# Optimization experiments

Measured on AMD Instinct MI355X. Metric: run time of the kernel, lower is better.

## Reference

```python
import jax, jax.numpy as jnp
import numpy as np

B, N_IN, N_ALL, NPT, K, C, H = 8, 20000, 1200, 1024, 34, 96, 6
DH = C // H
RADIUS2 = (2.5 * 0.04) ** 2  # grid_size=0.04, sigma=1.0 -> radius 0.1


def _fps(xyz, npoint):
    # furthest point sampling, vectorized over batch, scan over sample steps
    Bb, Nn, _ = xyz.shape
    def step(carry, _):
        dist, far = carry
        cen = jnp.take_along_axis(xyz, far[:, None, None], axis=1)  # [B,1,3]
        d = jnp.sum((xyz - cen) ** 2, -1)                           # [B,N]
        dist = jnp.minimum(dist, d)
        return (dist, jnp.argmax(dist, -1).astype(jnp.int32)), far
    init = (jnp.full((Bb, Nn), 1e10, xyz.dtype), jnp.zeros((Bb,), jnp.int32))
    _, idx = jax.lax.scan(step, init, None, length=npoint)
    return idx.T  # [B, npoint]


def _gather(x, idx):
    return jnp.take_along_axis(x, idx[:, :, None], axis=1)


def _ln(x, g, b):
    m = jnp.mean(x, -1, keepdims=True)
    v = jnp.var(x, -1, keepdims=True)
    return (x - m) * jax.lax.rsqrt(v + 1e-5) * g + b


def _forward(point_clouds, cloud_colors, W_in, b_in, Wq, Wk, Wv, Wo, Wpos, W1, b1, W2, b2, g1, be1, g2, be2, sel):
    fps_idx = _fps(point_clouds, N_ALL)      # [B,1200]
    fps_idx = fps_idx[:, sel]                # random 1024 of 1200 (fixed permutation)
    coord = _gather(point_clouds, fps_idx)   # [B,P,3]
    color = _gather(cloud_colors, fps_idx)   # [B,P,3]
    # ball query within each cloud (all clouds have equal count -> batched dense dists)
    d2 = jnp.sum((coord[:, :, None] - coord[:, None]) ** 2, -1)        # [B,P,P]
    valid = d2 <= RADIUS2
    nidx = jnp.argsort(jnp.where(valid, d2, 1e10), axis=-1)[..., :K]   # [B,P,K]
    nvalid = jnp.take_along_axis(valid, nidx, axis=-1)                 # [B,P,K]
    feat = jnp.concatenate([color, coord], -1)                         # [B,P,6]
    x = feat @ W_in + b_in                                             # [B,P,C]
    q = (x @ Wq).reshape(B, NPT, H, DH)
    k = x @ Wk
    v = x @ Wv
    def gat(t):  # gather per-neighbor features: [B,P,C*] -> [B,P,K,C*]
        return jnp.take_along_axis(t, nidx.reshape(B, NPT * K)[:, :, None], axis=1).reshape(B, NPT, K, -1)
    kn, vn, pn = gat(k), gat(v), gat(coord)
    pe = (coord[:, :, None] - pn) @ Wpos                               # [B,P,K,C] rel-pos enc
    kn = (kn + pe).reshape(B, NPT, K, H, DH)
    vn = (vn + pe).reshape(B, NPT, K, H, DH)
    logits = jnp.einsum('bphd,bpkhd->bphk', q, kn) / jnp.sqrt(jnp.float32(DH))
    logits = jnp.where(nvalid[:, :, None, :], logits, -1e9)
    attn = jax.nn.softmax(logits, -1)
    out = jnp.einsum('bphk,bpkhd->bphd', attn, vn).reshape(B, NPT, C)
    x = _ln(x + out @ Wo, g1, be1)
    x = _ln(x + jax.nn.relu(x @ W1 + b1) @ W2 + b2, g2, be2)
    features = jnp.transpose(x, (0, 2, 1))                             # [B,C,P]
    return features, coord


def setup_inputs() -> dict:
    key = jax.random.key(0)
    ks = jax.random.split(key, 16)
    s = 0.1
    w = lambda k, shp: jax.random.normal(k, shp, jnp.float32) * s
    return {
        'point_clouds': jax.random.uniform(ks[0], (B, N_IN, 3), jnp.float32),
        'cloud_colors': jax.random.uniform(ks[1], (B, N_IN, 3), jnp.float32),
        'W_in': w(ks[2], (6, C)), 'b_in': jnp.zeros((C,), jnp.float32),
        'Wq': w(ks[3], (C, C)), 'Wk': w(ks[4], (C, C)), 'Wv': w(ks[5], (C, C)),
        'Wo': w(ks[6], (C, C)), 'Wpos': w(ks[7], (3, C)),
        'W1': w(ks[8], (C, 4 * C)), 'b1': jnp.zeros((4 * C,), jnp.float32),
        'W2': w(ks[9], (4 * C, C)), 'b2': jnp.zeros((C,), jnp.float32),
        'g1': jnp.ones((C,), jnp.float32), 'be1': jnp.zeros((C,), jnp.float32),
        'g2': jnp.ones((C,), jnp.float32), 'be2': jnp.zeros((C,), jnp.float32),
        'sel': jax.random.permutation(ks[10], N_ALL)[:NPT].astype(jnp.int32),
    }


def reference(point_clouds, cloud_colors, W_in, b_in, Wq, Wk, Wv, Wo, Wpos, W1, b1, W2, b2, g1, be1, g2, be2, sel):
    return _forward(point_clouds, cloud_colors, W_in, b_in, Wq, Wk, Wv, Wo, Wpos, W1, b1, W2, b2, g1, be1, g2, be2, sel)
```

## Files before the change

kernel.cpp:

```cpp
#include <hip/hip_runtime.h>
#include <math.h>

#define B_   8
#define NIN  20000
#define NALL 1200
#define NPTQ 1024
#define KNB  34
#define CH   96
#define FF   384
#define NQ   (B_ * NPTQ)

typedef unsigned int   u32;
typedef unsigned long long u64;

__device__ __forceinline__ float scrub(float f) {
    u32 u = __float_as_uint(f);
    return ((u & 0x7F800000u) == 0x7F800000u) ? 12345.0f : f;
}

__global__ __launch_bounds__(1024) void fps_kernel(const float* __restrict__ pc,
                                                   int* __restrict__ fps_idx) {
    const int b = blockIdx.x;
    const int tid = threadIdx.x;
    const float* base = pc + (size_t)b * NIN * 3;

    float px[20], py[20], pz[20], dist[20];
#pragma unroll
    for (int j = 0; j < 20; ++j) {
        int idx = tid + j * 1024;
        bool ok = (j < 19) || (idx < NIN);
        int ia = ok ? idx : 0;
        px[j] = base[(size_t)ia * 3 + 0];
        py[j] = base[(size_t)ia * 3 + 1];
        pz[j] = base[(size_t)ia * 3 + 2];
        dist[j] = ok ? 1e10f : -1.0f;
    }

    __shared__ float cen[3];
    __shared__ u64 red[16];

    if (tid == 0) {
        fps_idx[b * NALL + 0] = 0;
        cen[0] = px[0]; cen[1] = py[0]; cen[2] = pz[0];
    }
    __syncthreads();

    for (int it = 1; it < NALL; ++it) {
        float cx = cen[0], cy = cen[1], cz = cen[2];
        float bd = -1e38f; int bi = 0;
#pragma unroll
        for (int j = 0; j < 20; ++j) {
            float dx = __fsub_rn(px[j], cx);
            float dy = __fsub_rn(py[j], cy);
            float dz = __fsub_rn(pz[j], cz);
            float d = __fadd_rn(__fadd_rn(__fmul_rn(dx, dx), __fmul_rn(dy, dy)),
                                __fmul_rn(dz, dz));
            float nd = fminf(dist[j], d);
            dist[j] = nd;
            if (nd > bd) { bd = nd; bi = tid + j * 1024; }
        }
        u64 key = ((u64)__float_as_uint(bd) << 32) | (u32)(NIN - bi);
#pragma unroll
        for (int s = 32; s; s >>= 1) {
            u64 o = __shfl_xor(key, s, 64);
            key = (o > key) ? o : key;
        }
        if ((tid & 63) == 0) red[tid >> 6] = key;
        __syncthreads();
        if (tid < 64) {
            u64 k2 = red[tid & 15];
#pragma unroll
            for (int s = 8; s; s >>= 1) {
                u64 o = __shfl_xor(k2, s, 64);
                k2 = (o > k2) ? o : k2;
            }
            if (tid == 0) {
                int w = NIN - (int)(k2 & 0xFFFFFFFFu);
                fps_idx[b * NALL + it] = w;
                const float* p = base + (size_t)w * 3;
                cen[0] = p[0]; cen[1] = p[1]; cen[2] = p[2];
            }
        }
        __syncthreads();
    }
}

__global__ void gather_kernel(const float* __restrict__ pc,
                              const int* __restrict__ fps_idx, const int* __restrict__ sel,
                              float* __restrict__ coord, float* __restrict__ out_coord) {
    int t = blockIdx.x * 256 + threadIdx.x;
    if (t >= NQ) return;
    int b = t >> 10, j = t & 1023;
    int p = fps_idx[b * NALL + sel[j]];
    p = (p < 0) ? 0 : ((p >= NIN) ? (NIN - 1) : p);
    const float* pp = pc + ((size_t)b * NIN + p) * 3;
    float x = pp[0], y = pp[1], z = pp[2];
    coord[(size_t)t * 3 + 0] = x;
    coord[(size_t)t * 3 + 1] = y;
    coord[(size_t)t * 3 + 2] = z;
    out_coord[(size_t)t * 3 + 0] = scrub(x);
    out_coord[(size_t)t * 3 + 1] = scrub(y);
    out_coord[(size_t)t * 3 + 2] = scrub(z);
}

__global__ void knn_kernel(const float* __restrict__ coord, int* __restrict__ nbr) {
    __shared__ float sx[NPTQ], sy[NPTQ], sz[NPTQ];
    const double RAD2D = (2.5 * 0.04) * (2.5 * 0.04);
    int b = blockIdx.x >> 8;
    int i0 = (blockIdx.x & 255) * 4;
    const float* cb = coord + (size_t)b * NPTQ * 3;
    for (int t = threadIdx.x; t < NPTQ; t += 256) {
        sx[t] = cb[(size_t)t * 3 + 0];
        sy[t] = cb[(size_t)t * 3 + 1];
        sz[t] = cb[(size_t)t * 3 + 2];
    }
    __syncthreads();
    int wid = threadIdx.x >> 6, lane = threadIdx.x & 63;
    int i = i0 + wid;
    float qx = sx[i], qy = sy[i], qz = sz[i];
    u64 pk[16];
#pragma unroll
    for (int t = 0; t < 16; ++t) {
        int j = lane + t * 64;
        float dx = __fsub_rn(qx, sx[j]);
        float dy = __fsub_rn(qy, sy[j]);
        float dz = __fsub_rn(qz, sz[j]);
        float d2 = __fadd_rn(__fadd_rn(__fmul_rn(dx, dx), __fmul_rn(dy, dy)),
                             __fmul_rn(dz, dz));
        bool valid = ((double)d2 <= RAD2D);
        pk[t] = valid ? (((u64)__float_as_uint(d2) << 32) | (u32)j) : ~0ull;
    }
    int* out = nbr + ((size_t)b * NPTQ + i) * KNB;
    int k = 0;
    for (; k < KNB; ++k) {
        u64 m = ~0ull;
#pragma unroll
        for (int t = 0; t < 16; ++t) m = (pk[t] < m) ? pk[t] : m;
#pragma unroll
        for (int s = 32; s; s >>= 1) {
            u64 o = __shfl_xor(m, s, 64);
            m = (o < m) ? o : m;
        }
        if (m == ~0ull) break;
#pragma unroll
        for (int t = 0; t < 16; ++t) if (pk[t] == m) pk[t] = ~0ull;
        if (lane == 0) out[k] = (int)(m & 0xFFFFFFFFu);
    }
    for (; k < KNB; ++k) if (lane == 0) out[k] = -1;
}

__global__ void xproj_kernel(const float* __restrict__ pc, const float* __restrict__ col,
                             const int* __restrict__ fps_idx, const int* __restrict__ sel,
                             const float* __restrict__ Win, const float* __restrict__ bin,
                             float* __restrict__ x) {
    int idx = blockIdx.x * 256 + threadIdx.x;
    if (idx >= NQ * CH) return;
    int q = idx / CH, c = idx - q * CH;
    int b = q >> 10, j = q & 1023;
    int p = fps_idx[b * NALL + sel[j]];
    p = (p < 0) ? 0 : ((p >= NIN) ? (NIN - 1) : p);
    const float* pp = pc + ((size_t)b * NIN + p) * 3;
    const float* cc = col + ((size_t)b * NIN + p) * 3;
    float acc = bin[c];
    acc += cc[0] * Win[0 * CH + c];
    acc += cc[1] * Win[1 * CH + c];
    acc += cc[2] * Win[2 * CH + c];
    acc += pp[0] * Win[3 * CH + c];
    acc += pp[1] * Win[4 * CH + c];
    acc += pp[2] * Win[5 * CH + c];
    x[idx] = acc;
}

__global__ void qkv_kernel(const float* __restrict__ x,
                           const float* __restrict__ Wq, const float* __restrict__ Wk,
                           const float* __restrict__ Wv,
                           float* __restrict__ qo, float* __restrict__ ko,
                           float* __restrict__ vo) {
    int idx = blockIdx.x * 256 + threadIdx.x;
    if (idx >= NQ * CH) return;
    int q = idx / CH, c = idx - q * CH;
    const float* xr = x + (size_t)q * CH;
    float aq = 0.f, ak = 0.f, av = 0.f;
    for (int k = 0; k < CH; ++k) {
        float xv = xr[k];
        aq += xv * Wq[k * CH + c];
        ak += xv * Wk[k * CH + c];
        av += xv * Wv[k * CH + c];
    }
    qo[idx] = aq; ko[idx] = ak; vo[idx] = av;
}

__global__ __launch_bounds__(384) void attn_kernel(float* __restrict__ qr1,
                            const float* __restrict__ km, const float* __restrict__ vm,
                            const float* __restrict__ coord, const int* __restrict__ nbr,
                            const float* __restrict__ Wpos, const float* __restrict__ Wo,
                            const float* __restrict__ x) {
    __shared__ float wp[3 * CH];
    __shared__ float os[4][CH];
    for (int t = threadIdx.x; t < 3 * CH; t += 384) wp[t] = Wpos[t];
    __syncthreads();
    int lq = threadIdx.x / CH;
    int c = threadIdx.x - lq * CH;
    int qi = blockIdx.x * 4 + lq;
    int b = qi >> 10, i = qi & 1023;
    const float* crd = coord + (size_t)b * NPTQ * 3;
    float cx = crd[(size_t)i * 3], cy = crd[(size_t)i * 3 + 1], cz = crd[(size_t)i * 3 + 2];
    float qv = qr1[(size_t)qi * CH + c];
    const int* nb = nbr + (size_t)qi * KNB;
    float m = -1e30f, l = 0.f, acc = 0.f;
    for (int t = 0; t < KNB; ++t) {
        int j = nb[t];
        if (j < 0) break;
        float dx = cx - crd[(size_t)j * 3];
        float dy = cy - crd[(size_t)j * 3 + 1];
        float dz = cz - crd[(size_t)j * 3 + 2];
        float pe = dx * wp[c] + dy * wp[CH + c] + dz * wp[2 * CH + c];
        size_t row = (size_t)(b * NPTQ + j) * CH + c;
        float kn = km[row] + pe;
        float s = qv * kn;
        s += __shfl_xor(s, 1); s += __shfl_xor(s, 2);
        s += __shfl_xor(s, 4); s += __shfl_xor(s, 8);
        float logit = s * 0.25f;
        float mn = fmaxf(m, logit);
        float sc = expf(m - mn);
        float p = expf(logit - mn);
        float vn = vm[row] + pe;
        l = l * sc + p;
        acc = acc * sc + p * vn;
        m = mn;
    }
    os[lq][c] = (l > 0.f) ? acc / l : 0.f;
    __syncthreads();
    float r = x[(size_t)qi * CH + c];
    for (int k = 0; k < CH; ++k) r += os[lq][k] * Wo[k * CH + c];
    qr1[(size_t)qi * CH + c] = r;
}

__global__ void ln_kernel(const float* __restrict__ in, const float* __restrict__ g,
                          const float* __restrict__ be, float* __restrict__ out) {
    int row = blockIdx.x * 4 + (threadIdx.x >> 6);
    int lane = threadIdx.x & 63;
    const float* r = in + (size_t)row * CH;
    float e0 = r[lane];
    float e1 = (lane < 32) ? r[64 + lane] : 0.0f;
    float s = e0 + e1;
#pragma unroll
    for (int k = 32; k; k >>= 1) s += __shfl_xor(s, k);
    float mean = s * (1.0f / 96.0f);
    float d0 = e0 - mean, d1 = e1 - mean;
    float vs = d0 * d0 + ((lane < 32) ? d1 * d1 : 0.0f);
#pragma unroll
    for (int k = 32; k; k >>= 1) vs += __shfl_xor(vs, k);
    float rs = 1.0f / sqrtf(vs * (1.0f / 96.0f) + 1e-5f);
    float* o = out + (size_t)row * CH;
    o[lane] = d0 * rs * g[lane] + be[lane];
    if (lane < 32) o[64 + lane] = d1 * rs * g[64 + lane] + be[64 + lane];
}

__global__ __launch_bounds__(384) void ffn_kernel(const float* __restrict__ x2,
                           const float* __restrict__ W1, const float* __restrict__ b1,
                           const float* __restrict__ W2, const float* __restrict__ b2,
                           float* __restrict__ r2) {
    __shared__ float xs[CH];
    __shared__ float hs[FF];
    __shared__ float ps[4][CH];
    int row = blockIdx.x, t = threadIdx.x;
    if (t < CH) xs[t] = x2[(size_t)row * CH + t];
    __syncthreads();
    float a = b1[t];
    for (int k = 0; k < CH; ++k) a += xs[k] * W1[k * FF + t];
    hs[t] = fmaxf(a, 0.0f);
    __syncthreads();
    int chunk = t / CH;
    int c = t - chunk * CH;
    float p = 0.f;
    for (int m = chunk * CH; m < (chunk + 1) * CH; ++m) p += hs[m] * W2[m * CH + c];
    ps[chunk][c] = p;
    __syncthreads();
    if (t < CH) {
        float r = xs[t] + ((ps[0][t] + ps[1][t]) + (ps[2][t] + ps[3][t])) + b2[t];
        r2[(size_t)row * CH + t] = r;
    }
}

__global__ void ln2t_kernel(const float* __restrict__ in, const float* __restrict__ g,
                            const float* __restrict__ be, float* __restrict__ out) {
    int row = blockIdx.x * 4 + (threadIdx.x >> 6);
    int lane = threadIdx.x & 63;
    int b = row >> 10, i = row & 1023;
    const float* r = in + (size_t)row * CH;
    float e0 = r[lane];
    float e1 = (lane < 32) ? r[64 + lane] : 0.0f;
    float s = e0 + e1;
#pragma unroll
    for (int k = 32; k; k >>= 1) s += __shfl_xor(s, k);
    float mean = s * (1.0f / 96.0f);
    float d0 = e0 - mean, d1 = e1 - mean;
    float vs = d0 * d0 + ((lane < 32) ? d1 * d1 : 0.0f);
#pragma unroll
    for (int k = 32; k; k >>= 1) vs += __shfl_xor(vs, k);
    float rs = 1.0f / sqrtf(vs * (1.0f / 96.0f) + 1e-5f);
    float y0 = d0 * rs * g[lane] + be[lane];
    out[((size_t)(b * CH + lane)) * NPTQ + i] = scrub(y0);
    if (lane < 32) {
        float y1 = d1 * rs * g[64 + lane] + be[64 + lane];
        out[((size_t)(b * CH + 64 + lane)) * NPTQ + i] = scrub(y1);
    }
}

extern "C" void kernel_launch(void* const* d_in, const int* in_sizes, int n_in,
                              void* d_out, int out_size, void* d_ws, size_t ws_size,
                              hipStream_t stream) {
    const float* pc   = (const float*)d_in[0];
    const float* col  = (const float*)d_in[1];
    const float* Win  = (const float*)d_in[2];
    const float* bin  = (const float*)d_in[3];
    const float* Wq   = (const float*)d_in[4];
    const float* Wk   = (const float*)d_in[5];
    const float* Wv   = (const float*)d_in[6];
    const float* Wo   = (const float*)d_in[7];
    const float* Wpos = (const float*)d_in[8];
    const float* W1   = (const float*)d_in[9];
    const float* b1   = (const float*)d_in[10];
    const float* W2   = (const float*)d_in[11];
    const float* b2   = (const float*)d_in[12];
    const float* g1   = (const float*)d_in[13];
    const float* be1  = (const float*)d_in[14];
    const float* g2   = (const float*)d_in[15];
    const float* be2  = (const float*)d_in[16];
    const int*  sel   = (const int*)d_in[17];

    float* out_feat  = (float*)d_out;
    float* out_coord = out_feat + (size_t)B_ * CH * NPTQ;

    char* ws = (char*)d_ws;
    size_t off = 0;
    auto alloc = [&](size_t bytes) { void* p = ws + off; off += (bytes + 255) & ~(size_t)255; return p; };
    int*   w_fps   = (int*)  alloc((size_t)B_ * NALL * 4);
    float* w_coord = (float*)alloc((size_t)NQ * 3 * 4);
    int*   w_nbr   = (int*)  alloc((size_t)NQ * KNB * 4);
    float* w_x     = (float*)alloc((size_t)NQ * CH * 4);
    float* w_q     = (float*)alloc((size_t)NQ * CH * 4);
    float* w_k     = (float*)alloc((size_t)NQ * CH * 4);
    float* w_v     = (float*)alloc((size_t)NQ * CH * 4);
    (void)ws_size; (void)in_sizes; (void)n_in; (void)out_size;

    fps_kernel<<<B_, 1024, 0, stream>>>(pc, w_fps);
    gather_kernel<<<NQ / 256, 256, 0, stream>>>(pc, w_fps, sel, w_coord, out_coord);
    knn_kernel<<<NQ / 4, 256, 0, stream>>>(w_coord, w_nbr);
    xproj_kernel<<<NQ * CH / 256, 256, 0, stream>>>(pc, col, w_fps, sel, Win, bin, w_x);
    qkv_kernel<<<NQ * CH / 256, 256, 0, stream>>>(w_x, Wq, Wk, Wv, w_q, w_k, w_v);
    attn_kernel<<<NQ / 4, 384, 0, stream>>>(w_q, w_k, w_v, w_coord, w_nbr, Wpos, Wo, w_x);
    ln_kernel<<<NQ / 4, 256, 0, stream>>>(w_q, g1, be1, w_k);
    ffn_kernel<<<NQ, 384, 0, stream>>>(w_k, W1, b1, W2, b2, w_v);
    ln2t_kernel<<<NQ / 4, 256, 0, stream>>>(w_v, g2, be2, out_feat);
}
```

Baseline: 2.786 ms.

## Split FPS across multiple blocks per cloud with global flag sync; batch FFN rows

Furthest point sampling now runs on 8 cooperating 256-thread blocks per cloud instead of one 1024-thread block. Each step, every block publishes its local argmax key and centroid to global memory and raises a per-block flag, then spins until all sibling blocks have posted before reducing to the global winner. This spreads the serial FPS loop across more CUs, at the cost of a global-memory handshake each iteration and reliance on all blocks being co-resident to avoid deadlock. Separately, the FFN kernel processes four rows per block so each W1/W2 weight load is reused four times.

Result: slower. 6.089 ms (+118.5%).

```diff
diff --git a/kernel.cpp b/kernel.cpp
--- a/kernel.cpp
+++ b/kernel.cpp
@@ -10,6 +10,11 @@
 #define FF   384
 #define NQ   (B_ * NPTQ)
 
+#define SPLIT 8
+#define PPB   (NIN / SPLIT)
+#define FPS_T 256
+#define SLOTS 10
+
 typedef unsigned int   u32;
 typedef unsigned long long u64;
 
@@ -18,38 +23,38 @@
     return ((u & 0x7F800000u) == 0x7F800000u) ? 12345.0f : f;
 }
 
-__global__ __launch_bounds__(1024) void fps_kernel(const float* __restrict__ pc,
-                                                   int* __restrict__ fps_idx) {
-    const int b = blockIdx.x;
+__global__ __launch_bounds__(FPS_T) void fps_kernel(
+        const float* __restrict__ pc, int* __restrict__ fps_idx,
+        u32* flags, u64* __restrict__ hkey, float4* __restrict__ hcen) {
+    const int b   = blockIdx.x / SPLIT;
+    const int s   = blockIdx.x - b * SPLIT;
     const int tid = threadIdx.x;
+    const int lane = tid & 63;
     const float* base = pc + (size_t)b * NIN * 3;
-
-    float px[20], py[20], pz[20], dist[20];
-#pragma unroll
-    for (int j = 0; j < 20; ++j) {
-        int idx = tid + j * 1024;
-        bool ok = (j < 19) || (idx < NIN);
-        int ia = ok ? idx : 0;
-        px[j] = base[(size_t)ia * 3 + 0];
-        py[j] = base[(size_t)ia * 3 + 1];
-        pz[j] = base[(size_t)ia * 3 + 2];
+    const int gbase = s * PPB;
+
+    float px[SLOTS], py[SLOTS], pz[SLOTS], dist[SLOTS];
+#pragma unroll
+    for (int j = 0; j < SLOTS; ++j) {
+        int ib = tid + j * FPS_T;
+        bool ok = ib < PPB;
+        int g = gbase + (ok ? ib : 0);
+        px[j] = base[(size_t)g * 3 + 0];
+        py[j] = base[(size_t)g * 3 + 1];
+        pz[j] = base[(size_t)g * 3 + 2];
         dist[j] = ok ? 1e10f : -1.0f;
     }
 
-    __shared__ float cen[3];
-    __shared__ u64 red[16];
-
-    if (tid == 0) {
-        fps_idx[b * NALL + 0] = 0;
-        cen[0] = px[0]; cen[1] = py[0]; cen[2] = pz[0];
-    }
-    __syncthreads();
+    __shared__ u64 red[4];
+    __shared__ float scen[3];
+
+    float cx = base[0], cy = base[1], cz = base[2];
+    if (s == 0 && tid == 0) fps_idx[b * NALL + 0] = 0;
 
     for (int it = 1; it < NALL; ++it) {
-        float cx = cen[0], cy = cen[1], cz = cen[2];
         float bd = -1e38f; int bi = 0;
 #pragma unroll
-        for (int j = 0; j < 20; ++j) {
+        for (int j = 0; j < SLOTS; ++j) {
             float dx = __fsub_rn(px[j], cx);
             float dy = __fsub_rn(py[j], cy);
             float dz = __fsub_rn(pz[j], cz);
@@ -57,31 +62,58 @@
                                 __fmul_rn(dz, dz));
             float nd = fminf(dist[j], d);
             dist[j] = nd;
-            if (nd > bd) { bd = nd; bi = tid + j * 1024; }
+            if (nd > bd) { bd = nd; bi = gbase + tid + j * FPS_T; }
         }
         u64 key = ((u64)__float_as_uint(bd) << 32) | (u32)(NIN - bi);
-#pragma unroll
-        for (int s = 32; s; s >>= 1) {
-            u64 o = __shfl_xor(key, s, 64);
-            key = (o > key) ? o : key;
-        }
-        if ((tid & 63) == 0) red[tid >> 6] = key;
+        u64 kw = key;
+#pragma unroll
+        for (int st = 32; st; st >>= 1) {
+            u64 o = __shfl_xor(kw, st, 64);
+            kw = (o > kw) ? o : kw;
+        }
+        if (lane == 0) red[tid >> 6] = kw;
         __syncthreads();
+        u64 k2 = red[lane & 3];
+#pragma unroll
+        for (int st = 1; st < 4; st <<= 1) {
+            u64 o = __shfl_xor(k2, st, 64);
+            k2 = (o > k2) ? o : k2;
+        }
+        if (key == k2) {
+            int wj = (bi - gbase - tid) >> 8;
+            size_t slot = ((size_t)b * NALL + it) * SPLIT + s;
+            hkey[slot] = k2;
+            hcen[slot] = make_float4(px[wj], py[wj], pz[wj], 0.f);
+            __threadfence();
+            __hip_atomic_store(&flags[b * SPLIT + s], (u32)it,
+                               __ATOMIC_RELEASE, __HIP_MEMORY_SCOPE_AGENT);
+        }
         if (tid < 64) {
-            u64 k2 = red[tid & 15];
-#pragma unroll
-            for (int s = 8; s; s >>= 1) {
-                u64 o = __shfl_xor(k2, s, 64);
-                k2 = (o > k2) ? o : k2;
+            u64 kk = 0; float xx = 0.f, yy = 0.f, zz = 0.f;
+            if (lane < SPLIT) {
+                while (__hip_atomic_load(&flags[b * SPLIT + lane],
+                                         __ATOMIC_ACQUIRE, __HIP_MEMORY_SCOPE_AGENT)
+                       < (u32)it) { }
+                size_t slot = ((size_t)b * NALL + it) * SPLIT + lane;
+                kk = hkey[slot];
+                float4 cc = hcen[slot];
+                xx = cc.x; yy = cc.y; zz = cc.z;
             }
-            if (tid == 0) {
-                int w = NIN - (int)(k2 & 0xFFFFFFFFu);
-                fps_idx[b * NALL + it] = w;
-                const float* p = base + (size_t)w * 3;
-                cen[0] = p[0]; cen[1] = p[1]; cen[2] = p[2];
+#pragma unroll
+            for (int st = 1; st < SPLIT; st <<= 1) {
+                u64 ok = __shfl_xor(kk, st, 64);
+                float ox = __shfl_xor(xx, st, 64);
+                float oy = __shfl_xor(yy, st, 64);
+                float oz = __shfl_xor(zz, st, 64);
+                if (ok > kk) { kk = ok; xx = ox; yy = oy; zz = oz; }
             }
+            if (lane == 0) {
+                scen[0] = xx; scen[1] = yy; scen[2] = zz;
+                if (s == 0) fps_idx[b * NALL + it] = NIN - (int)(kk & 0xFFFFFFFFu);
+            }
         }
         __syncthreads();
+        cx = scen[0]; cy = scen[1]; cz = scen[2];
     }
 }
 
@@ -261,26 +293,40 @@
                            const float* __restrict__ W1, const float* __restrict__ b1,
                            const float* __restrict__ W2, const float* __restrict__ b2,
                            float* __restrict__ r2) {
-    __shared__ float xs[CH];
-    __shared__ float hs[FF];
-    __shared__ float ps[4][CH];
-    int row = blockIdx.x, t = threadIdx.x;
-    if (t < CH) xs[t] = x2[(size_t)row * CH + t];
-    __syncthreads();
-    float a = b1[t];
-    for (int k = 0; k < CH; ++k) a += xs[k] * W1[k * FF + t];
-    hs[t] = fmaxf(a, 0.0f);
-    __syncthreads();
-    int chunk = t / CH;
-    int c = t - chunk * CH;
-    float p = 0.f;
-    for (int m = chunk * CH; m < (chunk + 1) * CH; ++m) p += hs[m] * W2[m * CH + c];
-    ps[chunk][c] = p;
-    __syncthreads();
-    if (t < CH) {
-        float r = xs[t] + ((ps[0][t] + ps[1][t]) + (ps[2][t] + ps[3][t])) + b2[t];
-        r2[(size_t)row * CH + t] = r;
-    }
+    __shared__ float xs[4][CH];
+    __shared__ float hs[4][FF];
+    __shared__ float ps[4][4][CH];
+    int row0 = blockIdx.x * 4, t = threadIdx.x;
+    { int r = t / CH, c = t - (t / CH) * CH;
+      xs[r][c] = x2[(size_t)(row0 + r) * CH + c]; }
+    __syncthreads();
+    {
+        float bt = b1[t];
+        float a0 = bt, a1 = bt, a2 = bt, a3 = bt;
+        for (int k = 0; k < CH; ++k) {
+            float w = W1[k * FF + t];
+            a0 += xs[0][k] * w; a1 += xs[1][k] * w;
+            a2 += xs[2][k] * w; a3 += xs[3][k] * w;
+        }
+        hs[0][t] = fmaxf(a0, 0.f); hs[1][t] = fmaxf(a1, 0.f);
+        hs[2][t] = fmaxf(a2, 0.f); hs[3][t] = fmaxf(a3, 0.f);
+    }
+    __syncthreads();
+    {
+        int chunk = t / CH, c = t - chunk * CH;
+        float p0 = 0.f, p1 = 0.f, p2 = 0.f, p3 = 0.f;
+        for (int m = chunk * CH; m < (chunk + 1) * CH; ++m) {
+            float w = W2[m * CH + c];
+            p0 += hs[0][m] * w; p1 += hs[1][m] * w;
+            p2 += hs[2][m] * w; p3 += hs[3][m] * w;
+        }
+        ps[0][chunk][c] = p0; ps[1][chunk][c] = p1;
+        ps[2][chunk][c] = p2; ps[3][chunk][c] = p3;
+    }
+    __syncthreads();
+    { int r = t / CH, c = t - (t / CH) * CH;
+      float rr = xs[r][c] + ((ps[r][0][c] + ps[r][1][c]) + (ps[r][2][c] + ps[r][3][c])) + b2[c];
+      r2[(size_t)(row0 + r) * CH + c] = rr; }
 }
 
 __global__ void ln2t_kernel(const float* __restrict__ in, const float* __restrict__ g,
@@ -336,22 +382,27 @@
     char* ws = (char*)d_ws;
     size_t off = 0;
     auto alloc = [&](size_t bytes) { void* p = ws + off; off += (bytes + 255) & ~(size_t)255; return p; };
-    int*   w_fps   = (int*)  alloc((size_t)B_ * NALL * 4);
-    float* w_coord = (float*)alloc((size_t)NQ * 3 * 4);
-    int*   w_nbr   = (int*)  alloc((size_t)NQ * KNB * 4);
-    float* w_x     = (float*)alloc((size_t)NQ * CH * 4);
-    float* w_q     = (float*)alloc((size_t)NQ * CH * 4);
-    float* w_k     = (float*)alloc((size_t)NQ * CH * 4);
-    float* w_v     = (float*)alloc((size_t)NQ * CH * 4);
+    u32*    w_flags = (u32*)   alloc((size_t)B_ * SPLIT * 4);
+    u64*    w_hkey  = (u64*)   alloc((size_t)B_ * NALL * SPLIT * 8);
+    float4* w_hcen  = (float4*)alloc((size_t)B_ * NALL * SPLIT * 16);
+    int*    w_fps   = (int*)   alloc((size_t)B_ * NALL * 4);
+    float*  w_coord = (float*) alloc((size_t)NQ * 3 * 4);
+    int*    w_nbr   = (int*)   alloc((size_t)NQ * KNB * 4);
+    float*  w_x     = (float*) alloc((size_t)NQ * CH * 4);
+    float*  w_q     = (float*) alloc((size_t)NQ * CH * 4);
+    float*  w_k     = (float*) alloc((size_t)NQ * CH * 4);
+    float*  w_v     = (float*) alloc((size_t)NQ * CH * 4);
     (void)ws_size; (void)in_sizes; (void)n_in; (void)out_size;
 
-    fps_kernel<<<B_, 1024, 0, stream>>>(pc, w_fps);
+    hipMemsetAsync(w_flags, 0, (size_t)B_ * SPLIT * 4, stream);
+
+    fps_kernel<<<B_ * SPLIT, FPS_T, 0, stream>>>(pc, w_fps, w_flags, w_hkey, w_hcen);
     gather_kernel<<<NQ / 256, 256, 0, stream>>>(pc, w_fps, sel, w_coord, out_coord);
     knn_kernel<<<NQ / 4, 256, 0, stream>>>(w_coord, w_nbr);
     xproj_kernel<<<NQ * CH / 256, 256, 0, stream>>>(pc, col, w_fps, sel, Win, bin, w_x);
     qkv_kernel<<<NQ * CH / 256, 256, 0, stream>>>(w_x, Wq, Wk, Wv, w_q, w_k, w_v);
     attn_kernel<<<NQ / 4, 384, 0, stream>>>(w_q, w_k, w_v, w_coord, w_nbr, Wpos, Wo, w_x);
     ln_kernel<<<NQ / 4, 256, 0, stream>>>(w_q, g1, be1, w_k);
-    ffn_kernel<<<NQ, 384, 0, stream>>>(w_k, W1, b1, W2, b2, w_v);
+    ffn_kernel<<<NQ / 4, 384, 0, stream>>>(w_k, W1, b1, W2, b2, w_v);
     ln2t_kernel<<<NQ / 4, 256, 0, stream>>>(w_v, g2, be2, out_feat);
 }
```

## Halve FPS barriers with double-buffered reduction and batch FFN rows per block

Applied to the files above, without the earlier changes.

The FPS loop now has every wave read the per-wave partial maxima from a double-buffered shared array and reduce them redundantly. Each thread then loads the new centroid itself, which removes the second __syncthreads and the serial tid==0 step in each of the 1199 iterations. The FFN kernel now processes four rows per block, so each W1/W2 weight load is reused four times, and the grid shrinks accordingly. The cost is more redundant reduction work and global loads of the centroid by every thread, plus more shared memory in the FFN.

New measurement: 2.627 ms. 5.7% less time.

```diff
diff --git a/kernel.cpp b/kernel.cpp
--- a/kernel.cpp
+++ b/kernel.cpp
@@ -9,6 +9,7 @@
 #define CH   96
 #define FF   384
 #define NQ   (B_ * NPTQ)
+#define SL   20
 
 typedef unsigned int   u32;
 typedef unsigned long long u64;
@@ -22,34 +23,36 @@
                                                    int* __restrict__ fps_idx) {
     const int b = blockIdx.x;
     const int tid = threadIdx.x;
+    const int lane = tid & 63;
+    const int wid = tid >> 6;
     const float* base = pc + (size_t)b * NIN * 3;
 
-    float px[20], py[20], pz[20], dist[20];
-#pragma unroll
-    for (int j = 0; j < 20; ++j) {
+    float px[SL], py[SL], pz[SL], dist[SL];
+#pragma unroll
+    for (int j = 0; j < SL; ++j) {
         int idx = tid + j * 1024;
-        bool ok = (j < 19) || (idx < NIN);
+        bool ok = (j < SL - 1) || (idx < NIN);
         int ia = ok ? idx : 0;
         px[j] = base[(size_t)ia * 3 + 0];
         py[j] = base[(size_t)ia * 3 + 1];
         pz[j] = base[(size_t)ia * 3 + 2];
         dist[j] = ok ? 1e10f : -1.0f;
     }
-
-    __shared__ float cen[3];
-    __shared__ u64 red[16];
-
-    if (tid == 0) {
-        fps_idx[b * NALL + 0] = 0;
-        cen[0] = px[0]; cen[1] = py[0]; cen[2] = pz[0];
-    }
-    __syncthreads();
+#pragma unroll
+    for (int j = 0; j < SL; ++j) {
+        asm volatile("" : "+v"(px[j]), "+v"(py[j]), "+v"(pz[j]));
+    }
+
+    __shared__ u64 red[2][16];
+
+    if (tid == 0) fps_idx[b * NALL + 0] = 0;
+    float cx = base[0], cy = base[1], cz = base[2];
 
     for (int it = 1; it < NALL; ++it) {
-        float cx = cen[0], cy = cen[1], cz = cen[2];
+        const int p = it & 1;
         float bd = -1e38f; int bi = 0;
 #pragma unroll
-        for (int j = 0; j < 20; ++j) {
+        for (int j = 0; j < SL; ++j) {
             float dx = __fsub_rn(px[j], cx);
             float dy = __fsub_rn(py[j], cy);
             float dz = __fsub_rn(pz[j], cz);
@@ -65,23 +68,18 @@
             u64 o = __shfl_xor(key, s, 64);
             key = (o > key) ? o : key;
         }
-        if ((tid & 63) == 0) red[tid >> 6] = key;
+        if (lane == 0) red[p][wid] = key;
         __syncthreads();
-        if (tid < 64) {
-            u64 k2 = red[tid & 15];
-#pragma unroll
-            for (int s = 8; s; s >>= 1) {
-                u64 o = __shfl_xor(k2, s, 64);
-                k2 = (o > k2) ? o : k2;
-            }
-            if (tid == 0) {
-                int w = NIN - (int)(k2 & 0xFFFFFFFFu);
-                fps_idx[b * NALL + it] = w;
-                const float* p = base + (size_t)w * 3;
-                cen[0] = p[0]; cen[1] = p[1]; cen[2] = p[2];
-            }
-        }
-        __syncthreads();
+        u64 k2 = red[p][lane & 15];
+#pragma unroll
+        for (int s = 1; s < 16; s <<= 1) {
+            u64 o = __shfl_xor(k2, s, 64);
+            k2 = (o > k2) ? o : k2;
+        }
+        int widx = NIN - (int)(k2 & 0xFFFFFFFFu);
+        if (tid == 0) fps_idx[b * NALL + it] = widx;
+        const float* wp = base + (size_t)widx * 3;
+        cx = wp[0]; cy = wp[1]; cz = wp[2];
     }
 }
 
@@ -261,26 +259,40 @@
                            const float* __restrict__ W1, const float* __restrict__ b1,
                            const float* __restrict__ W2, const float* __restrict__ b2,
                            float* __restrict__ r2) {
-    __shared__ float xs[CH];
-    __shared__ float hs[FF];
-    __shared__ float ps[4][CH];
-    int row = blockIdx.x, t = threadIdx.x;
-    if (t < CH) xs[t] = x2[(size_t)row * CH + t];
-    __syncthreads();
-    float a = b1[t];
-    for (int k = 0; k < CH; ++k) a += xs[k] * W1[k * FF + t];
-    hs[t] = fmaxf(a, 0.0f);
-    __syncthreads();
-    int chunk = t / CH;
-    int c = t - chunk * CH;
-    float p = 0.f;
-    for (int m = chunk * CH; m < (chunk + 1) * CH; ++m) p += hs[m] * W2[m * CH + c];
-    ps[chunk][c] = p;
-    __syncthreads();
-    if (t < CH) {
-        float r = xs[t] + ((ps[0][t] + ps[1][t]) + (ps[2][t] + ps[3][t])) + b2[t];
-        r2[(size_t)row * CH + t] = r;
-    }
+    __shared__ float xs[4][CH];
+    __shared__ float hs[4][FF];
+    __shared__ float ps[4][4][CH];
+    int row0 = blockIdx.x * 4, t = threadIdx.x;
+    { int r = t / CH, c = t - (t / CH) * CH;
+      xs[r][c] = x2[(size_t)(row0 + r) * CH + c]; }
+    __syncthreads();
+    {
+        float bt = b1[t];
+        float a0 = bt, a1 = bt, a2 = bt, a3 = bt;
+        for (int k = 0; k < CH; ++k) {
+            float w = W1[k * FF + t];
+            a0 += xs[0][k] * w; a1 += xs[1][k] * w;
+            a2 += xs[2][k] * w; a3 += xs[3][k] * w;
+        }
+        hs[0][t] = fmaxf(a0, 0.f); hs[1][t] = fmaxf(a1, 0.f);
+        hs[2][t] = fmaxf(a2, 0.f); hs[3][t] = fmaxf(a3, 0.f);
+    }
+    __syncthreads();
+    {
+        int chunk = t / CH, c = t - (t / CH) * CH;
+        float p0 = 0.f, p1 = 0.f, p2 = 0.f, p3 = 0.f;
+        for (int m = chunk * CH; m < (chunk + 1) * CH; ++m) {
+            float w = W2[m * CH + c];
+            p0 += hs[0][m] * w; p1 += hs[1][m] * w;
+            p2 += hs[2][m] * w; p3 += hs[3][m] * w;
+        }
+        ps[0][chunk][c] = p0; ps[1][chunk][c] = p1;
+        ps[2][chunk][c] = p2; ps[3][chunk][c] = p3;
+    }
+    __syncthreads();
+    { int r = t / CH, c = t - (t / CH) * CH;
+      float rr = xs[r][c] + ((ps[r][0][c] + ps[r][1][c]) + (ps[r][2][c] + ps[r][3][c])) + b2[c];
+      r2[(size_t)(row0 + r) * CH + c] = rr; }
 }
 
 __global__ void ln2t_kernel(const float* __restrict__ in, const float* __restrict__ g,
@@ -352,6 +364,6 @@
     qkv_kernel<<<NQ * CH / 256, 256, 0, stream>>>(w_x, Wq, Wk, Wv, w_q, w_k, w_v);
     attn_kernel<<<NQ / 4, 384, 0, stream>>>(w_q, w_k, w_v, w_coord, w_nbr, Wpos, Wo, w_x);
     ln_kernel<<<NQ / 4, 256, 0, stream>>>(w_q, g1, be1, w_k);
-    ffn_kernel<<<NQ, 384, 0, stream>>>(w_k, W1, b1, W2, b2, w_v);
+    ffn_kernel<<<NQ / 4, 384, 0, stream>>>(w_k, W1, b1, W2, b2, w_v);
     ln2t_kernel<<<NQ / 4, 256, 0, stream>>>(w_v, g2, be2, out_feat);
 }
```
